# Kernel tuning notes

Hardware: AMD Instinct MI355X
Metric: run time of the kernel (lower is better)

## Reference

```python
import jax, jax.numpy as jnp
import numpy as np

B, N, D = 32768, 256, 3


def setup_inputs() -> dict:
    key = jax.random.key(0)
    k1, k2 = jax.random.split(key)
    keypoints = jax.random.normal(k1, (B, N, D), dtype=jnp.float32)
    perm = jax.random.permutation(k2, B)  # emulates torch.randperm, deterministic
    return {"keypoints": keypoints, "perm": perm}


def _transform_a2b(src, dst):
    # src, dst: [B, N, 3]; batched similarity (Umeyama/Kabsch-style) alignment.
    num = src.shape[1]
    src_mean = src.mean(axis=1)                     # [B, 3]
    dst_mean = dst.mean(axis=1)                     # [B, 3]
    src_d = src - src_mean[:, None]                 # [B, N, 3]
    dst_d = dst - dst_mean[:, None]                 # [B, N, 3]
    A = jnp.einsum('bni,bnj->bij', dst_d, src_d) / num  # [B, 3, 3] covariance
    U, S, Vt = jnp.linalg.svd(A)
    # NOTE: in the original torch code `d[neg_A][:, -1, -1] = -1` writes into a
    # COPY (advanced indexing), so d stays identity for all batches. We
    # faithfully reproduce that actual behavior: R = U @ V^T, scale uses sum(S).
    var_sum = jnp.mean(jnp.sum(src_d * src_d, axis=-1), axis=1)  # sum of per-dim biased var
    scale = jnp.sum(S, axis=-1) / var_sum           # [B]
    R = U @ Vt                                      # [B, 3, 3]
    T = dst_mean - scale[:, None] * jnp.einsum('bij,bj->bi', R, src_mean)  # [B, 3]
    # Original computes R, scale, T under torch.no_grad().
    R = jax.lax.stop_gradient(R)
    scale = jax.lax.stop_gradient(scale)
    T = jax.lax.stop_gradient(T)
    return src @ (jnp.swapaxes(R, -1, -2) * scale[:, None, None]) + T[:, None]


def reference(keypoints, perm):
    dst = keypoints[perm]                            # randomized keypoints
    trans = _transform_a2b(keypoints, dst)
    return jnp.mean(jnp.abs(trans - dst))
```

## Files before the change

kernel.cpp:

```cpp
#include <hip/hip_runtime.h>
#include <math.h>

#define GEO_N 256

__device__ __forceinline__ float frcp(float x) { return __builtin_amdgcn_rcpf(x); }
__device__ __forceinline__ float frsq(float x) { return __builtin_amdgcn_rsqf(x); }
__device__ __forceinline__ float fsqrtf_(float x) { return __builtin_amdgcn_sqrtf(x); }

__device__ __forceinline__ float wredf(float v) {
#pragma unroll
  for (int off = 32; off; off >>= 1) v += __shfl_xor(v, off, 64);
  return v;
}

template <int P, int Q>
__device__ __forceinline__ void jrot(float G[3][3], float V[3][3]) {
  const float apq = G[P][Q];
  const float tau = (G[Q][Q] - G[P][P]) * 0.5f * frcp(apq);
  const float tt = fsqrtf_(1.0f + tau * tau);
  const float tr = frcp(tau + copysignf(tt, tau));
  const float cr = frsq(1.0f + tr * tr);
  const bool skip = fabsf(apq) < 1e-30f;
  const float c = skip ? 1.0f : cr;
  const float s = skip ? 0.0f : tr * cr;
#pragma unroll
  for (int k = 0; k < 3; ++k) {
    float gkp = G[k][P], gkq = G[k][Q];
    G[k][P] = c * gkp - s * gkq;
    G[k][Q] = s * gkp + c * gkq;
  }
#pragma unroll
  for (int k = 0; k < 3; ++k) {
    float gpk = G[P][k], gqk = G[Q][k];
    G[P][k] = c * gpk - s * gqk;
    G[Q][k] = s * gpk + c * gqk;
  }
#pragma unroll
  for (int k = 0; k < 3; ++k) {
    float vkp = V[k][P], vkq = V[k][Q];
    V[k][P] = c * vkp - s * vkq;
    V[k][Q] = s * vkp + c * vkq;
  }
}

__device__ __forceinline__ void solve_rst(const float s0[16], float bc[13]) {
  const float invN = 1.0f / (float)GEO_N;
  const float smx = s0[0] * invN, smy = s0[1] * invN, smz = s0[2] * invN;
  const float dmx = s0[3] * invN, dmy = s0[4] * invN, dmz = s0[5] * invN;
  float A[3][3];
  A[0][0] = s0[6] * invN - dmx * smx;  A[0][1] = s0[7] * invN - dmx * smy;  A[0][2] = s0[8] * invN - dmx * smz;
  A[1][0] = s0[9] * invN - dmy * smx;  A[1][1] = s0[10] * invN - dmy * smy; A[1][2] = s0[11] * invN - dmy * smz;
  A[2][0] = s0[12] * invN - dmz * smx; A[2][1] = s0[13] * invN - dmz * smy; A[2][2] = s0[14] * invN - dmz * smz;
  const float var_sum = s0[15] * invN - (smx * smx + smy * smy + smz * smz);

  float G[3][3];
#pragma unroll
  for (int i = 0; i < 3; ++i)
#pragma unroll
    for (int j = 0; j < 3; ++j)
      G[i][j] = A[0][i] * A[0][j] + A[1][i] * A[1][j] + A[2][i] * A[2][j];
  float V[3][3] = {{1, 0, 0}, {0, 1, 0}, {0, 0, 1}};
#pragma unroll
  for (int sweep = 0; sweep < 4; ++sweep) {
    jrot<0, 1>(G, V);
    jrot<0, 2>(G, V);
    jrot<1, 2>(G, V);
  }
  float l0 = G[0][0], l1 = G[1][1], l2 = G[2][2];
  if (l0 < l1) { float tl = l0; l0 = l1; l1 = tl;
#pragma unroll
    for (int k = 0; k < 3; ++k) { float tv = V[k][0]; V[k][0] = V[k][1]; V[k][1] = tv; } }
  if (l0 < l2) { float tl = l0; l0 = l2; l2 = tl;
#pragma unroll
    for (int k = 0; k < 3; ++k) { float tv = V[k][0]; V[k][0] = V[k][2]; V[k][2] = tv; } }
  if (l1 < l2) { float tl = l1; l1 = l2; l2 = tl;
#pragma unroll
    for (int k = 0; k < 3; ++k) { float tv = V[k][1]; V[k][1] = V[k][2]; V[k][2] = tv; } }
  const float sig0 = fsqrtf_(fmaxf(l0, 0.0f));
  const float sig1 = fsqrtf_(fmaxf(l1, 0.0f));
  const float sig2 = fsqrtf_(fmaxf(l2, 0.0f));

  float v0[3] = {V[0][0], V[1][0], V[2][0]};
  float v1[3] = {V[0][1], V[1][1], V[2][1]};
  float v2[3] = {V[0][2], V[1][2], V[2][2]};
  float u0[3], u1[3], u2r[3];
#pragma unroll
  for (int i = 0; i < 3; ++i) {
    u0[i]  = A[i][0] * v0[0] + A[i][1] * v0[1] + A[i][2] * v0[2];
    u1[i]  = A[i][0] * v1[0] + A[i][1] * v1[1] + A[i][2] * v1[2];
    u2r[i] = A[i][0] * v2[0] + A[i][1] * v2[1] + A[i][2] * v2[2];
  }
  float n0 = u0[0] * u0[0] + u0[1] * u0[1] + u0[2] * u0[2];
  if (n0 > 1e-28f) { float inv = frsq(n0); u0[0] *= inv; u0[1] *= inv; u0[2] *= inv; }
  else { u0[0] = 1.0f; u0[1] = 0.0f; u0[2] = 0.0f; }
  float d01 = u1[0] * u0[0] + u1[1] * u0[1] + u1[2] * u0[2];
  u1[0] -= d01 * u0[0]; u1[1] -= d01 * u0[1]; u1[2] -= d01 * u0[2];
  float n1 = u1[0] * u1[0] + u1[1] * u1[1] + u1[2] * u1[2];
  if (n1 > 1e-28f) { float inv = frsq(n1); u1[0] *= inv; u1[1] *= inv; u1[2] *= inv; }
  else {
    float ex[3] = {1, 0, 0}, ey[3] = {0, 1, 0};
    const float* e = (fabsf(u0[0]) < 0.9f) ? ex : ey;
    u1[0] = u0[1] * e[2] - u0[2] * e[1];
    u1[1] = u0[2] * e[0] - u0[0] * e[2];
    u1[2] = u0[0] * e[1] - u0[1] * e[0];
    float nn = u1[0] * u1[0] + u1[1] * u1[1] + u1[2] * u1[2];
    float inv = frsq(nn);
    u1[0] *= inv; u1[1] *= inv; u1[2] *= inv;
  }
  float u2[3] = {u0[1] * u1[2] - u0[2] * u1[1],
                 u0[2] * u1[0] - u0[0] * u1[2],
                 u0[0] * u1[1] - u0[1] * u1[0]};
  float d2 = u2[0] * u2r[0] + u2[1] * u2r[1] + u2[2] * u2r[2];
  if (d2 < 0.0f) { u2[0] = -u2[0]; u2[1] = -u2[1]; u2[2] = -u2[2]; }

  const float scale = (sig0 + sig1 + sig2) * frcp(fmaxf(var_sum, 1e-30f));
  float R[3][3];
#pragma unroll
  for (int i = 0; i < 3; ++i)
#pragma unroll
    for (int j = 0; j < 3; ++j)
      R[i][j] = u0[i] * v0[j] + u1[i] * v1[j] + u2[i] * v2[j];
  const float Tx = dmx - scale * (R[0][0] * smx + R[0][1] * smy + R[0][2] * smz);
  const float Ty = dmy - scale * (R[1][0] * smx + R[1][1] * smy + R[1][2] * smz);
  const float Tz = dmz - scale * (R[2][0] * smx + R[2][1] * smy + R[2][2] * smz);
#pragma unroll
  for (int i = 0; i < 3; ++i)
#pragma unroll
    for (int j = 0; j < 3; ++j) bc[3 * i + j] = R[i][j];
  bc[9] = scale; bc[10] = Tx; bc[11] = Ty; bc[12] = Tz;
}

__global__ __launch_bounds__(256) void geo_wave4t(const float* __restrict__ kp,
                                                  const int* __restrict__ perm,
                                                  float* __restrict__ partials,
                                                  int B, int NW) {
  const int wid = (blockIdx.x << 2) | (threadIdx.x >> 6);
  if (wid >= NW) return;
  const int lane = threadIdx.x & 63;
  const int g = lane >> 4, q = lane & 15;
  const int b0 = wid * 4;
  const int bi = b0 + g;
  const int bb = min(bi, B - 1);
  const float4* base = (const float4*)kp;

  const int pm = perm[bb];

  const float4* s4 = base + (size_t)bb * 192 + q * 12;
  const float4* d4 = base + (size_t)pm * 192 + q * 12;
  float4 S[12], D[12];
#pragma unroll
  for (int j = 0; j < 12; ++j) S[j] = s4[j];
#pragma unroll
  for (int j = 0; j < 12; ++j) D[j] = d4[j];

  float s[48], d[48];
#pragma unroll
  for (int j = 0; j < 12; ++j) {
    s[4 * j + 0] = S[j].x; s[4 * j + 1] = S[j].y; s[4 * j + 2] = S[j].z; s[4 * j + 3] = S[j].w;
    d[4 * j + 0] = D[j].x; d[4 * j + 1] = D[j].y; d[4 * j + 2] = D[j].z; d[4 * j + 3] = D[j].w;
  }

  float r[16];
#pragma unroll
  for (int k = 0; k < 16; ++k) r[k] = 0.0f;
#pragma unroll
  for (int p = 0; p < 16; ++p) {
    const float sx = s[3 * p + 0], sy = s[3 * p + 1], sz = s[3 * p + 2];
    const float dx = d[3 * p + 0], dy = d[3 * p + 1], dz = d[3 * p + 2];
    r[0] += sx; r[1] += sy; r[2] += sz;
    r[3] += dx; r[4] += dy; r[5] += dz;
    r[6] += dx * sx; r[7] += dx * sy; r[8] += dx * sz;
    r[9] += dy * sx; r[10] += dy * sy; r[11] += dy * sz;
    r[12] += dz * sx; r[13] += dz * sy; r[14] += dz * sz;
    r[15] += sx * sx + sy * sy + sz * sz;
  }

  const int b1 = q & 1, b2 = (q >> 1) & 1, b3 = (q >> 2) & 1, b4 = (q >> 3) & 1;
  float v8[8], v4[4], v2[2], parked;
#pragma unroll
  for (int k = 0; k < 8; ++k) {
    float send = b1 ? r[k] : r[k + 8];
    float recv = __shfl_xor(send, 1, 64);
    v8[k] = (b1 ? r[k + 8] : r[k]) + recv;
  }
#pragma unroll
  for (int k = 0; k < 4; ++k) {
    float send = b2 ? v8[k] : v8[k + 4];
    float recv = __shfl_xor(send, 2, 64);
    v4[k] = (b2 ? v8[k + 4] : v8[k]) + recv;
  }
#pragma unroll
  for (int k = 0; k < 2; ++k) {
    float send = b3 ? v4[k] : v4[k + 2];
    float recv = __shfl_xor(send, 4, 64);
    v2[k] = (b3 ? v4[k + 2] : v4[k]) + recv;
  }
  {
    float send = b4 ? v2[0] : v2[1];
    float recv = __shfl_xor(send, 8, 64);
    parked = (b4 ? v2[1] : v2[0]) + recv;
  }

  constexpr int br[16] = {0, 8, 4, 12, 2, 10, 6, 14, 1, 9, 5, 13, 3, 11, 7, 15};
  float s0[16];
#pragma unroll
  for (int k = 0; k < 16; ++k)
    s0[k] = __shfl(parked, (lane & 0x30) | br[k], 64);

  float bc[13];
  solve_rst(s0, bc);

  float acc = 0.0f;
#pragma unroll
  for (int p = 0; p < 16; ++p) {
    const float sx = s[3 * p + 0], sy = s[3 * p + 1], sz = s[3 * p + 2];
    const float dx = d[3 * p + 0], dy = d[3 * p + 1], dz = d[3 * p + 2];
    const float e0 = bc[9] * (bc[0] * sx + bc[1] * sy + bc[2] * sz) + bc[10] - dx;
    const float e1 = bc[9] * (bc[3] * sx + bc[4] * sy + bc[5] * sz) + bc[11] - dy;
    const float e2 = bc[9] * (bc[6] * sx + bc[7] * sy + bc[8] * sz) + bc[12] - dz;
    acc += fabsf(e0) + fabsf(e1) + fabsf(e2);
  }
  if (bi >= B) acc = 0.0f;

  acc = wredf(acc);
  if (lane == 0) partials[wid] = acc;
}

__global__ __launch_bounds__(1024) void geo_fin(const float* __restrict__ partials,
                                                float* __restrict__ out, int n,
                                                double inv_total) {
  const int t = threadIdx.x;
  double acc = 0.0;
  for (int i = t; i < n; i += 1024) acc += (double)partials[i];
#pragma unroll
  for (int off = 32; off; off >>= 1) acc += __shfl_xor(acc, off, 64);
  __shared__ double sred[16];
  if ((t & 63) == 0) sred[t >> 6] = acc;
  __syncthreads();
  if (t == 0) {
    double tot = 0.0;
#pragma unroll
    for (int k = 0; k < 16; ++k) tot += sred[k];
    out[0] = (float)(tot * inv_total);
  }
}

extern "C" void kernel_launch(void* const* d_in, const int* in_sizes, int n_in,
                              void* d_out, int out_size, void* d_ws, size_t ws_size,
                              hipStream_t stream) {
  const float* kp = (const float*)d_in[0];
  const int* perm = (const int*)d_in[1];
  float* out = (float*)d_out;
  const int B = in_sizes[1];
  const double inv_total = 1.0 / ((double)B * (double)GEO_N * 3.0);

  const int NW = (B + 3) / 4;
  float* partials = (float*)d_ws;
  const int grid = (NW + 3) / 4;
  geo_wave4t<<<grid, 256, 0, stream>>>(kp, perm, partials, B, NW);
  geo_fin<<<1, 1024, 0, stream>>>(partials, out, NW, inv_total);
}
```

Baseline: 46.58 us.

## Stage batches through LDS for coalesced loads, two batches per wave

Each wave now handles two batches instead of four. It loads each 3 KB batch with fully coalesced float4 accesses across all 64 lanes, stages the data in shared memory, then has 32 lanes per batch read their 8 points back from LDS. This replaces the old per-lane strided 192-byte global reads, aiming for better memory coalescing. In exchange it adds 48 KB of LDS per block (which limits occupancy), one extra shuffle stage in the reduction, twice as many waves, and no barrier, which is safe only because each wave reads back only its own LDS slice.

```diff
diff --git a/kernel.cpp b/kernel.cpp
--- a/kernel.cpp
+++ b/kernel.cpp
@@ -130,41 +130,58 @@
   bc[9] = scale; bc[10] = Tx; bc[11] = Ty; bc[12] = Tz;
 }
 
-__global__ __launch_bounds__(256) void geo_wave4t(const float* __restrict__ kp,
+__global__ __launch_bounds__(256) void geo_wave2c(const float* __restrict__ kp,
                                                   const int* __restrict__ perm,
                                                   float* __restrict__ partials,
                                                   int B, int NW) {
-  const int wid = (blockIdx.x << 2) | (threadIdx.x >> 6);
+  __shared__ float4 lds4[3072];
+  const int tid = threadIdx.x;
+  const int w = tid >> 6, lane = tid & 63;
+  const int wid = blockIdx.x * 4 + w;
   if (wid >= NW) return;
-  const int lane = threadIdx.x & 63;
-  const int g = lane >> 4, q = lane & 15;
-  const int b0 = wid * 4;
-  const int bi = b0 + g;
-  const int bb = min(bi, B - 1);
+  const int g = lane >> 5, q = lane & 31;
+  const int b0 = wid * 2;
+  float4* wbuf = lds4 + w * 768;
   const float4* base = (const float4*)kp;
 
-  const int pm = perm[bb];
-
-  const float4* s4 = base + (size_t)bb * 192 + q * 12;
-  const float4* d4 = base + (size_t)pm * 192 + q * 12;
-  float4 S[12], D[12];
-#pragma unroll
-  for (int j = 0; j < 12; ++j) S[j] = s4[j];
-#pragma unroll
-  for (int j = 0; j < 12; ++j) D[j] = d4[j];
-
-  float s[48], d[48];
-#pragma unroll
-  for (int j = 0; j < 12; ++j) {
-    s[4 * j + 0] = S[j].x; s[4 * j + 1] = S[j].y; s[4 * j + 2] = S[j].z; s[4 * j + 3] = S[j].w;
-    d[4 * j + 0] = D[j].x; d[4 * j + 1] = D[j].y; d[4 * j + 2] = D[j].z; d[4 * j + 3] = D[j].w;
+  const int pm0 = perm[min(b0, B - 1)];
+  const int pm1 = perm[min(b0 + 1, B - 1)];
+  const int bs0 = min(b0, B - 1), bs1 = min(b0 + 1, B - 1);
+
+  float4 st[12];
+#pragma unroll
+  for (int c = 0; c < 3; ++c) {
+    st[c]     = base[(size_t)bs0 * 192 + c * 64 + lane];
+    st[3 + c] = base[(size_t)pm0 * 192 + c * 64 + lane];
+    st[6 + c] = base[(size_t)bs1 * 192 + c * 64 + lane];
+    st[9 + c] = base[(size_t)pm1 * 192 + c * 64 + lane];
+  }
+#pragma unroll
+  for (int c = 0; c < 3; ++c) {
+    wbuf[      c * 64 + lane] = st[c];
+    wbuf[192 + c * 64 + lane] = st[3 + c];
+    wbuf[384 + c * 64 + lane] = st[6 + c];
+    wbuf[576 + c * 64 + lane] = st[9 + c];
+  }
+
+  float4 SP[6], DP[6];
+#pragma unroll
+  for (int j = 0; j < 6; ++j) {
+    SP[j] = wbuf[g * 384 +       q * 6 + j];
+    DP[j] = wbuf[g * 384 + 192 + q * 6 + j];
+  }
+  float s[24], d[24];
+#pragma unroll
+  for (int j = 0; j < 6; ++j) {
+    s[4 * j + 0] = SP[j].x; s[4 * j + 1] = SP[j].y; s[4 * j + 2] = SP[j].z; s[4 * j + 3] = SP[j].w;
+    d[4 * j + 0] = DP[j].x; d[4 * j + 1] = DP[j].y; d[4 * j + 2] = DP[j].z; d[4 * j + 3] = DP[j].w;
   }
 
   float r[16];
 #pragma unroll
   for (int k = 0; k < 16; ++k) r[k] = 0.0f;
 #pragma unroll
-  for (int p = 0; p < 16; ++p) {
+  for (int p = 0; p < 8; ++p) {
     const float sx = s[3 * p + 0], sy = s[3 * p + 1], sz = s[3 * p + 2];
     const float dx = d[3 * p + 0], dy = d[3 * p + 1], dz = d[3 * p + 2];
     r[0] += sx; r[1] += sy; r[2] += sz;
@@ -176,7 +193,7 @@
   }
 
   const int b1 = q & 1, b2 = (q >> 1) & 1, b3 = (q >> 2) & 1, b4 = (q >> 3) & 1;
-  float v8[8], v4[4], v2[2], parked;
+  float v8[8], v4[4], v2[2], v1;
 #pragma unroll
   for (int k = 0; k < 8; ++k) {
     float send = b1 ? r[k] : r[k + 8];
@@ -198,21 +215,22 @@
   {
     float send = b4 ? v2[0] : v2[1];
     float recv = __shfl_xor(send, 8, 64);
-    parked = (b4 ? v2[1] : v2[0]) + recv;
-  }
+    v1 = (b4 ? v2[1] : v2[0]) + recv;
+  }
+  const float parked = v1 + __shfl_xor(v1, 16, 64);
 
   constexpr int br[16] = {0, 8, 4, 12, 2, 10, 6, 14, 1, 9, 5, 13, 3, 11, 7, 15};
   float s0[16];
 #pragma unroll
   for (int k = 0; k < 16; ++k)
-    s0[k] = __shfl(parked, (lane & 0x30) | br[k], 64);
+    s0[k] = __shfl(parked, (lane & 0x20) | br[k], 64);
 
   float bc[13];
   solve_rst(s0, bc);
 
   float acc = 0.0f;
 #pragma unroll
-  for (int p = 0; p < 16; ++p) {
+  for (int p = 0; p < 8; ++p) {
     const float sx = s[3 * p + 0], sy = s[3 * p + 1], sz = s[3 * p + 2];
     const float dx = d[3 * p + 0], dy = d[3 * p + 1], dz = d[3 * p + 2];
     const float e0 = bc[9] * (bc[0] * sx + bc[1] * sy + bc[2] * sz) + bc[10] - dx;
@@ -220,7 +238,7 @@
     const float e2 = bc[9] * (bc[6] * sx + bc[7] * sy + bc[8] * sz) + bc[12] - dz;
     acc += fabsf(e0) + fabsf(e1) + fabsf(e2);
   }
-  if (bi >= B) acc = 0.0f;
+  if (b0 + g >= B) acc = 0.0f;
 
   acc = wredf(acc);
   if (lane == 0) partials[wid] = acc;
@@ -254,9 +272,9 @@
   const int B = in_sizes[1];
   const double inv_total = 1.0 / ((double)B * (double)GEO_N * 3.0);
 
-  const int NW = (B + 3) / 4;
+  const int NW = (B + 1) / 2;
   float* partials = (float*)d_ws;
   const int grid = (NW + 3) / 4;
-  geo_wave4t<<<grid, 256, 0, stream>>>(kp, perm, partials, B, NW);
+  geo_wave2c<<<grid, 256, 0, stream>>>(kp, perm, partials, B, NW);
   geo_fin<<<1, 1024, 0, stream>>>(partials, out, NW, inv_total);
 }
```

After: 47.96 us. 1.03x slower.
